# Kernel optimization log

Measured on AMD Instinct MI355X. Metric: run time of the kernel, lower is better.

The kernel has to match this reference:

```python
import jax, jax.numpy as jnp
import numpy as np

B, VOCAB, HIST, PEN_RANGE = 256, 128000, 512, 64


def setup_inputs() -> dict:
    key = jax.random.key(0)
    k1, k2, k3 = jax.random.split(key, 3)
    logits = jax.random.normal(k1, (B, VOCAB), dtype=jnp.float32)
    save_id = jax.random.randint(k2, (B, HIST), 0, VOCAB, dtype=jnp.int64)
    penalty_value = jax.random.uniform(k3, (1,), dtype=jnp.float32)
    return {
        "logits": logits,
        "save_id": save_id,
        "penalty_value": penalty_value,
        "penalty_range": PEN_RANGE,
    }


def reference(logits, save_id, penalty_value, penalty_range):
    # target_indices = save_id[:, -penalty_range:]  -> [B, R]
    idx = save_id[:, -penalty_range:]
    # gather logits at idx, multiply by penalty, scatter back (out-of-place)
    penalized = jnp.take_along_axis(logits, idx, axis=1) * penalty_value  # [B, R]
    rows = jnp.arange(logits.shape[0])[:, None]  # [B, 1]
    return logits.at[rows, idx].set(penalized)
```

## Files before the change

kernel.cpp:

```cpp
#include <hip/hip_runtime.h>

#define VOCAB 128000
#define HIST 512

__global__ void APPLY_PENALTY_5909874999394_copy(const float4* __restrict__ in,
                                                 float4* __restrict__ out,
                                                 long n4) {
    long i = (long)blockIdx.x * blockDim.x + threadIdx.x;
    long stride = (long)gridDim.x * blockDim.x;
    for (; i < n4; i += stride) {
        out[i] = in[i];
    }
}

__global__ void APPLY_PENALTY_5909874999394_scatter(const float* __restrict__ logits,
                                                    const int* __restrict__ save_id,
                                                    const float* __restrict__ pval,
                                                    const int* __restrict__ prange,
                                                    float* __restrict__ out) {
    int row = blockIdx.x;
    int pr = *prange;
    float p = *pval;
    const int base = row * HIST + (HIST - pr);
    const long rowoff = (long)row * VOCAB;
    for (int k = threadIdx.x; k < pr; k += blockDim.x) {
        int idx = save_id[base + k];
        out[rowoff + idx] = logits[rowoff + idx] * p;
    }
}

extern "C" void kernel_launch(void* const* d_in, const int* in_sizes, int n_in,
                              void* d_out, int out_size, void* d_ws, size_t ws_size,
                              hipStream_t stream) {
    const float* logits  = (const float*)d_in[0];
    const int*   save_id = (const int*)d_in[1];
    const float* pval    = (const float*)d_in[2];
    const int*   prange  = (const int*)d_in[3];
    float* out = (float*)d_out;

    long n4 = (long)out_size / 4;
    int block = 256;
    int grid = 2048;
    APPLY_PENALTY_5909874999394_copy<<<grid, block, 0, stream>>>(
        (const float4*)logits, (float4*)out, n4);

    int rows = out_size / VOCAB;
    APPLY_PENALTY_5909874999394_scatter<<<rows, 64, 0, stream>>>(
        logits, save_id, pval, prange, out);
}
```

Measured before the change: 47.78 us.

## Fuse row copy and penalty scatter into one per-row kernel

Replaces the separate grid-stride copy kernel and the scatter kernel with a single kernel that uses one 1024-thread block per row. Each block copies its row with vector loads and nontemporal stores, waits on a barrier, then applies the penalty scatter to that row. This removes one kernel launch and the gap between the two kernels, and the nontemporal stores are meant to keep the streamed output from polluting the cache. In exchange, parallelism is fixed at one block per row, and correctness depends on the barrier ordering the nontemporal stores before the scatter writes to the same addresses.

```diff
diff --git a/kernel.cpp b/kernel.cpp
--- a/kernel.cpp
+++ b/kernel.cpp
@@ -2,29 +2,34 @@
 
 #define VOCAB 128000
 #define HIST 512
+#define ROW_F4 (VOCAB / 4)
 
-__global__ void APPLY_PENALTY_5909874999394_copy(const float4* __restrict__ in,
-                                                 float4* __restrict__ out,
-                                                 long n4) {
-    long i = (long)blockIdx.x * blockDim.x + threadIdx.x;
-    long stride = (long)gridDim.x * blockDim.x;
-    for (; i < n4; i += stride) {
-        out[i] = in[i];
+typedef float f32x4 __attribute__((ext_vector_type(4)));
+
+__global__ __launch_bounds__(1024)
+void APPLY_PENALTY_5909874999394_fused(const f32x4* __restrict__ logits4,
+                                       const float* __restrict__ logits,
+                                       const int* __restrict__ save_id,
+                                       const float* __restrict__ pval,
+                                       const int* __restrict__ prange,
+                                       f32x4* __restrict__ out4,
+                                       float* __restrict__ out) {
+    const int row = blockIdx.x;
+    const long rowoff4 = (long)row * ROW_F4;
+
+    for (int j = threadIdx.x; j < ROW_F4; j += blockDim.x) {
+        f32x4 v = logits4[rowoff4 + j];
+        __builtin_nontemporal_store(v, &out4[rowoff4 + j]);
     }
-}
 
-__global__ void APPLY_PENALTY_5909874999394_scatter(const float* __restrict__ logits,
-                                                    const int* __restrict__ save_id,
-                                                    const float* __restrict__ pval,
-                                                    const int* __restrict__ prange,
-                                                    float* __restrict__ out) {
-    int row = blockIdx.x;
-    int pr = *prange;
-    float p = *pval;
+    __syncthreads();
+
+    const int pr = *prange;
+    const float p = *pval;
     const int base = row * HIST + (HIST - pr);
     const long rowoff = (long)row * VOCAB;
     for (int k = threadIdx.x; k < pr; k += blockDim.x) {
-        int idx = save_id[base + k];
+        const int idx = save_id[base + k];
         out[rowoff + idx] = logits[rowoff + idx] * p;
     }
 }
@@ -38,13 +43,8 @@
     const int*   prange  = (const int*)d_in[3];
     float* out = (float*)d_out;
 
-    long n4 = (long)out_size / 4;
-    int block = 256;
-    int grid = 2048;
-    APPLY_PENALTY_5909874999394_copy<<<grid, block, 0, stream>>>(
-        (const float4*)logits, (float4*)out, n4);
-
-    int rows = out_size / VOCAB;
-    APPLY_PENALTY_5909874999394_scatter<<<rows, 64, 0, stream>>>(
-        logits, save_id, pval, prange, out);
+    const int rows = out_size / VOCAB;
+    APPLY_PENALTY_5909874999394_fused<<<rows, 1024, 0, stream>>>(
+        (const f32x4*)logits, logits, save_id, pval, prange,
+        (f32x4*)out, out);
 }
```

After: 44.89 us. 1.06x faster.
